# Kernel optimization log

Hardware: AMD Instinct MI355X
Metric: run time of the kernel (lower is better)

Reference implementation:

```python
import jax, jax.numpy as jnp
import numpy as np
from jax.scipy.linalg import expm

B, T = 32, 4096
FREQ_DIM = 128
HID = 64
OUT_DIM = 2
N_COMP = 4
DT = 0.1
EPS = 1e-5


def setup_inputs() -> dict:
    key = jax.random.key(0)
    ks = jax.random.split(key, 16)
    f32 = jnp.float32

    def lin(k, out_d, in_d):
        bound = 1.0 / np.sqrt(in_d)
        kw, kb = jax.random.split(k)
        W = jax.random.uniform(kw, (out_d, in_d), f32, -bound, bound)
        b = jax.random.uniform(kb, (out_d,), f32, -bound, bound)
        return W, b

    x = jax.random.normal(ks[0], (B, T, 1), f32)
    # EnhancedWavePhysics params
    freq_spectrum = jnp.linspace(1.0, 20.0, FREQ_DIM, dtype=f32)
    pm_w1, pm_b1 = lin(ks[1], 128, 1)
    pm_w2, pm_b2 = lin(ks[2], FREQ_DIM * 2, 128)
    wc_w, wc_b = lin(ks[3], HID, FREQ_DIM)
    amp_ctrl = jnp.ones((1,), f32) * 0.1
    # quantum encoder
    qe_w1, qe_b1 = lin(ks[4], HID * 2, HID)
    qe_w2, qe_b2 = lin(ks[5], HID * 4, HID * 2)
    # layernorm
    ln_g = jnp.ones((HID * 4,), f32)
    ln_b = jnp.zeros((HID * 4,), f32)
    # skew-symmetric hamiltonians [4, 64, 64]
    A = jax.random.normal(ks[6], (N_COMP, HID, HID), f32) * 0.05
    hams = (A - jnp.swapaxes(A, -1, -2)) / 2.0
    # interference net
    int_w1, int_b1 = lin(ks[7], 32, 4)
    int_w2, int_b2 = lin(ks[8], OUT_DIM, 32)
    int_strength = jnp.ones((1,), f32)
    return dict(x=x, freq_spectrum=freq_spectrum, pm_w1=pm_w1, pm_b1=pm_b1,
                pm_w2=pm_w2, pm_b2=pm_b2, wc_w=wc_w, wc_b=wc_b,
                amp_ctrl=amp_ctrl, qe_w1=qe_w1, qe_b1=qe_b1, qe_w2=qe_w2,
                qe_b2=qe_b2, ln_g=ln_g, ln_b=ln_b, hams=hams,
                int_w1=int_w1, int_b1=int_b1, int_w2=int_w2, int_b2=int_b2,
                int_strength=int_strength)


def reference(x, freq_spectrum, pm_w1, pm_b1, pm_w2, pm_b2, wc_w, wc_b,
              amp_ctrl, qe_w1, qe_b1, qe_w2, qe_b2, ln_g, ln_b, hams,
              int_w1, int_b1, int_w2, int_b2, int_strength):
    Bx, Tx, _ = x.shape
    # --- EnhancedWavePhysics ---
    mod = jnp.tanh(x @ pm_w1.T + pm_b1) @ pm_w2.T + pm_b2            # [B,T,2F]
    amplitude, phase = jnp.split(mod, 2, axis=-1)                     # [B,T,F]
    amplitude = jnp.tanh(amplitude) * amp_ctrl
    time = jnp.linspace(0.0, 2.0 * np.pi, Tx)[None, :, None]          # [1,T,1]
    freqs = freq_spectrum[None, None, :]                              # [1,1,F]
    wave_components = amplitude * jnp.sin(freqs * time + phase)       # [B,T,F]
    wave_field = jnp.tanh(wave_components @ wc_w.T + wc_b)            # [B,T,H]
    # --- quantum encoder + layernorm ---
    q = jnp.tanh(wave_field @ qe_w1.T + qe_b1) @ qe_w2.T + qe_b2      # [B,T,4H]
    mu = q.mean(-1, keepdims=True)
    var = q.var(-1, keepdims=True)
    q = (q - mu) / jnp.sqrt(var + EPS) * ln_g + ln_b
    psi = q.reshape(Bx, Tx, N_COMP, HID)                              # [B,T,C,D]
    # --- Hamiltonian evolution: torch does matrix_exp(-1j*(1j*H)*dt)=expm(H*dt)
    #     (H skew-symmetric real => U real orthogonal), then psi @ U.T, take real.
    U = jax.vmap(expm)(hams * DT)                                     # [C,D,D]
    evolved = jnp.einsum('btcd,ced->btce', psi, U)                    # [B,T,C,D]
    # --- EnhancedInterference ---
    spec = jnp.abs(jnp.fft.fft(evolved, axis=1))                      # [B,T,C,D]
    freq_w = jax.nn.softmax(spec.mean(-1), axis=1)                    # [B,T,C]
    weighted = jnp.sum(spec * freq_w[..., None], axis=1)              # [B,C,D]
    spatial_avg = weighted.mean(-1)                                   # [B,C]
    out = jnp.tanh(spatial_avg @ int_w1.T + int_b1) @ int_w2.T + int_b2
    return out * int_strength                                         # [B,out_dim]
```

## Files before the change

kernel.cpp:

```cpp
#include <hip/hip_runtime.h>
#include <hip/hip_bf16.h>

#define TT 4096
#define BB 32

typedef unsigned short ushort_t;
typedef __attribute__((ext_vector_type(8))) short short8v;
typedef __attribute__((ext_vector_type(4))) float float4v;

__device__ inline ushort_t bf16rn(float v) {
    unsigned u = __float_as_uint(v);
    unsigned r = (u + 0x7FFFu + ((u >> 16) & 1u)) >> 16;
    return (ushort_t)r;
}
__device__ inline float bf16tof(ushort_t h) {
    return __uint_as_float(((unsigned)h) << 16);
}
__device__ inline int SW(int i) { return i + (i >> 5); }

__device__ inline float fast_tanh(float x) {
    float e = __builtin_amdgcn_exp2f(x * 2.8853900817779268f);
    return 1.0f - 2.0f * __builtin_amdgcn_rcpf(e + 1.0f);
}
__device__ inline float fast_sin(float x) {
    return __builtin_amdgcn_sinf(x * 0.15915494309189535f);
}

__global__ __launch_bounds__(256) void k1_expm(const float* __restrict__ hams,
                                               float* __restrict__ U)
{
    int c = blockIdx.x, tid = threadIdx.x;
    __shared__ float M[4096], P[4096], Acc[4096];
    const float* H = hams + c * 4096;
    for (int k = tid; k < 4096; k += 256) {
        float m = H[k] * 0.1f;
        M[k] = m; P[k] = m;
        Acc[k] = m + (((k >> 6) == (k & 63)) ? 1.0f : 0.0f);
    }
    __syncthreads();
    int j = tid & 63;
    float mcol[64];
    #pragma unroll
    for (int k = 0; k < 64; k++) mcol[k] = M[k * 64 + j];
    for (int term = 2; term <= 8; term++) {
        float inv = 1.0f / (float)term;
        float np_[16];
        #pragma unroll
        for (int r = 0; r < 16; r++) {
            int i = (tid >> 6) + 4 * r;
            float a = 0.f;
            #pragma unroll
            for (int k = 0; k < 64; k++) a = fmaf(P[i * 64 + k], mcol[k], a);
            np_[r] = a * inv;
        }
        __syncthreads();
        #pragma unroll
        for (int r = 0; r < 16; r++) {
            int i = (tid >> 6) + 4 * r;
            P[i * 64 + j] = np_[r];
            Acc[i * 64 + j] += np_[r];
        }
        __syncthreads();
    }
    for (int k = tid; k < 4096; k += 256) U[c * 4096 + k] = Acc[k];
}

__global__ void split_all(const float* __restrict__ pw2, const float* __restrict__ wcw,
                          const float* __restrict__ qw1, const float* __restrict__ qw2,
                          ushort_t* __restrict__ wb)
{
    int i = blockIdx.x * 256 + threadIdx.x;
    const float* src; ushort_t *hi, *lo; int off;
    if (i < 32768)      { src = pw2; hi = wb;          lo = wb + 32768;  off = i; }
    else if (i < 40960) { src = wcw; hi = wb + 65536;  lo = wb + 73728;  off = i - 32768; }
    else if (i < 49152) { src = qw1; hi = wb + 81920;  lo = wb + 90112;  off = i - 40960; }
    else                { src = qw2; hi = wb + 98304;  lo = wb + 131072; off = i - 49152; }
    float v = src[off];
    ushort_t h = bf16rn(v);
    hi[off] = h;
    lo[off] = bf16rn(v - bf16tof(h));
}

template<int EPI>
__global__ __launch_bounds__(256, 2) void gemm_v2(
    const ushort_t* __restrict__ Ahi, const ushort_t* __restrict__ Alo,
    const ushort_t* __restrict__ Whi, const ushort_t* __restrict__ Wlo,
    const float* __restrict__ bias,
    const float* __restrict__ x, const float* __restrict__ pw1,
    const float* __restrict__ pb1,
    const float* __restrict__ freq, const float* __restrict__ ampc,
    const float* __restrict__ lng, const float* __restrict__ lnb,
    ushort_t* __restrict__ OHi, ushort_t* __restrict__ OLo,
    float* __restrict__ OF)
{
    __shared__ float partS[2][4][16], partSS[2][4][16];
    int tid = threadIdx.x;
    int w = tid >> 6, l = tid & 63, l15 = l & 15, kg = l >> 4;
    int kofb = kg * 8;

    short8v bh[4][4], bl[4][4];
    #pragma unroll
    for (int i = 0; i < 4; i++) {
        int n = (w + 4 * i) * 16 + l15;
        #pragma unroll
        for (int kc = 0; kc < 4; kc++) {
            int kof = kc * 32 + kofb;
            bh[i][kc] = *(const short8v*)(Whi + (size_t)n * 128 + kof);
            bl[i][kc] = *(const short8v*)(Wlo + (size_t)n * 128 + kof);
        }
    }

    float fr[2], ba[2], bp[2], am = 0.f;
    float bv[4], g4[4], be4[4];
    if (EPI == 1) {
        am = ampc[0];
        #pragma unroll
        for (int i = 0; i < 2; i++) {
            int f = (w + 4 * i) * 16 + l15;
            fr[i] = freq[f]; ba[i] = bias[f]; bp[i] = bias[128 + f];
        }
    } else {
        #pragma unroll
        for (int i = 0; i < 4; i++) {
            int n = (w + 4 * i) * 16 + l15;
            bv[i] = bias[n]; g4[i] = lng[n]; be4[i] = lnb[n];
        }
    }

    int mbase = blockIdx.x * 256;
    for (int mi = 0; mi < 16; mi++) {
        int m0 = mbase + mi * 16;
        short8v ah[4], al[4];
        if (EPI == 1) {
            float xv = x[m0 + l15];
            #pragma unroll
            for (int kc = 0; kc < 4; kc++) {
                int k0 = kc * 32 + kofb;
                float4 w0 = *(const float4*)(pw1 + k0);
                float4 w1v = *(const float4*)(pw1 + k0 + 4);
                float4 b0 = *(const float4*)(pb1 + k0);
                float4 b1v = *(const float4*)(pb1 + k0 + 4);
                #pragma unroll
                for (int j = 0; j < 8; j++) {
                    float wj = (j < 4) ? (&w0.x)[j] : (&w1v.x)[j - 4];
                    float bj = (j < 4) ? (&b0.x)[j] : (&b1v.x)[j - 4];
                    float v = fast_tanh(fmaf(xv, wj, bj));
                    ushort_t h = bf16rn(v);
                    ah[kc][j] = (short)h;
                    al[kc][j] = (short)bf16rn(v - bf16tof(h));
                }
            }
        } else {
            #pragma unroll
            for (int kc = 0; kc < 4; kc++) {
                int kof = kc * 32 + kofb;
                ah[kc] = *(const short8v*)(Ahi + (size_t)(m0 + l15) * 128 + kof);
                al[kc] = *(const short8v*)(Alo + (size_t)(m0 + l15) * 128 + kof);
            }
        }

        float4v acc[4];
        #pragma unroll
        for (int i = 0; i < 4; i++) acc[i] = (float4v){0.f, 0.f, 0.f, 0.f};
        #pragma unroll
        for (int kc = 0; kc < 4; kc++) {
            #pragma unroll
            for (int i = 0; i < 4; i++) {
                acc[i] = __builtin_amdgcn_mfma_f32_16x16x32_bf16(ah[kc], bh[i][kc], acc[i], 0, 0, 0);
                acc[i] = __builtin_amdgcn_mfma_f32_16x16x32_bf16(ah[kc], bl[i][kc], acc[i], 0, 0, 0);
                acc[i] = __builtin_amdgcn_mfma_f32_16x16x32_bf16(al[kc], bh[i][kc], acc[i], 0, 0, 0);
            }
        }

        if (EPI == 1) {
            #pragma unroll
            for (int i = 0; i < 2; i++) {
                int f = (w + 4 * i) * 16 + l15;
                #pragma unroll
                for (int r = 0; r < 4; r++) {
                    int m = m0 + kg * 4 + r;
                    float timev = 6.283185307179586f * (float)(m & 4095) / 4095.0f;
                    float a = fast_tanh(acc[i][r] + ba[i]) * am;
                    float ph = acc[i + 2][r] + bp[i];
                    float v = a * fast_sin(fmaf(fr[i], timev, ph));
                    ushort_t h = bf16rn(v);
                    OHi[(size_t)m * 128 + f] = h;
                    OLo[(size_t)m * 128 + f] = bf16rn(v - bf16tof(h));
                }
            }
        } else {
            float s[4] = {0, 0, 0, 0}, ss[4] = {0, 0, 0, 0};
            #pragma unroll
            for (int i = 0; i < 4; i++) {
                #pragma unroll
                for (int r = 0; r < 4; r++) {
                    float v = acc[i][r] + bv[i];
                    s[r] += v; ss[r] += v * v;
                }
            }
            #pragma unroll
            for (int r = 0; r < 4; r++) {
                #pragma unroll
                for (int off = 1; off < 16; off <<= 1) {
                    s[r] += __shfl_xor(s[r], off);
                    ss[r] += __shfl_xor(ss[r], off);
                }
            }
            int pb_ = mi & 1;
            if (l15 == 0) {
                #pragma unroll
                for (int r = 0; r < 4; r++) {
                    partS[pb_][w][kg * 4 + r] = s[r];
                    partSS[pb_][w][kg * 4 + r] = ss[r];
                }
            }
            __syncthreads();
            float mu[4], rstd[4];
            #pragma unroll
            for (int r = 0; r < 4; r++) {
                float ts = 0.f, tss = 0.f;
                #pragma unroll
                for (int wv = 0; wv < 4; wv++) {
                    ts += partS[pb_][wv][kg * 4 + r];
                    tss += partSS[pb_][wv][kg * 4 + r];
                }
                mu[r] = ts * (1.0f / 256.0f);
                float var = tss * (1.0f / 256.0f) - mu[r] * mu[r];
                rstd[r] = rsqrtf(var + 1e-5f);
            }
            int b = m0 >> 12;
            int t0 = (m0 & 4095) + kg * 4;
            unsigned* OU = (unsigned*)OF;
            #pragma unroll
            for (int i = 0; i < 4; i++) {
                int n = (w + 4 * i) * 16 + l15;
                uint4 ov;
                #pragma unroll
                for (int r = 0; r < 4; r++) {
                    float v = (acc[i][r] + bv[i] - mu[r]) * rstd[r] * g4[i] + be4[i];
                    ushort_t h = bf16rn(v);
                    ushort_t lo2 = bf16rn(v - bf16tof(h));
                    (&ov.x)[r] = (unsigned)h | ((unsigned)lo2 << 16);
                }
                *(uint4*)(OU + (((size_t)b * 256 + n) << 12) + t0) = ov;
            }
        }
    }
}

__global__ __launch_bounds__(256, 2) void s23_v2(
    const ushort_t* __restrict__ Ahi, const ushort_t* __restrict__ Alo,
    const ushort_t* __restrict__ W2hi, const ushort_t* __restrict__ W2lo,
    const float* __restrict__ b2,
    const ushort_t* __restrict__ W3hi, const ushort_t* __restrict__ W3lo,
    const float* __restrict__ b3,
    ushort_t* __restrict__ OHi, ushort_t* __restrict__ OLo)
{
    __shared__ unsigned WF[2][16][65];
    int tid = threadIdx.x;
    int w = tid >> 6, l = tid & 63, l15 = l & 15, kg = l >> 4;
    int kofb = kg * 8;

    short8v w2h[4], w2l[4];
    #pragma unroll
    for (int kc = 0; kc < 4; kc++) {
        int n = w * 16 + l15;
        int kof = kc * 32 + kofb;
        w2h[kc] = *(const short8v*)(W2hi + (size_t)n * 128 + kof);
        w2l[kc] = *(const short8v*)(W2lo + (size_t)n * 128 + kof);
    }
    short8v w3h[2][2], w3l[2][2];
    #pragma unroll
    for (int i = 0; i < 2; i++) {
        int n = (w + 4 * i) * 16 + l15;
        #pragma unroll
        for (int kc = 0; kc < 2; kc++) {
            int kof = kc * 32 + kofb;
            w3h[i][kc] = *(const short8v*)(W3hi + (size_t)n * 64 + kof);
            w3l[i][kc] = *(const short8v*)(W3lo + (size_t)n * 64 + kof);
        }
    }
    float b2v = b2[w * 16 + l15];
    float b3v[2];
    #pragma unroll
    for (int i = 0; i < 2; i++) b3v[i] = b3[(w + 4 * i) * 16 + l15];

    int mbase = blockIdx.x * 256;
    for (int mi = 0; mi < 16; mi++) {
        int m0 = mbase + mi * 16;
        short8v ah[4], al[4];
        #pragma unroll
        for (int kc = 0; kc < 4; kc++) {
            int kof = kc * 32 + kofb;
            ah[kc] = *(const short8v*)(Ahi + (size_t)(m0 + l15) * 128 + kof);
            al[kc] = *(const short8v*)(Alo + (size_t)(m0 + l15) * 128 + kof);
        }
        float4v acc1 = (float4v){0.f, 0.f, 0.f, 0.f};
        #pragma unroll
        for (int kc = 0; kc < 4; kc++) {
            acc1 = __builtin_amdgcn_mfma_f32_16x16x32_bf16(ah[kc], w2h[kc], acc1, 0, 0, 0);
            acc1 = __builtin_amdgcn_mfma_f32_16x16x32_bf16(ah[kc], w2l[kc], acc1, 0, 0, 0);
            acc1 = __builtin_amdgcn_mfma_f32_16x16x32_bf16(al[kc], w2h[kc], acc1, 0, 0, 0);
        }
        int buf = mi & 1;
        #pragma unroll
        for (int r = 0; r < 4; r++) {
            float v = fast_tanh(acc1[r] + b2v);
            ushort_t h = bf16rn(v);
            ushort_t lo2 = bf16rn(v - bf16tof(h));
            WF[buf][kg * 4 + r][w * 16 + l15] = (unsigned)h | ((unsigned)lo2 << 16);
        }
        __syncthreads();
        float4v acc2[2];
        acc2[0] = (float4v){0.f, 0.f, 0.f, 0.f};
        acc2[1] = (float4v){0.f, 0.f, 0.f, 0.f};
        #pragma unroll
        for (int kc = 0; kc < 2; kc++) {
            short8v a2h, a2l;
            #pragma unroll
            for (int j = 0; j < 8; j++) {
                unsigned u = WF[buf][l15][kc * 32 + kofb + j];
                a2h[j] = (short)(u & 0xFFFFu);
                a2l[j] = (short)(u >> 16);
            }
            #pragma unroll
            for (int i = 0; i < 2; i++) {
                acc2[i] = __builtin_amdgcn_mfma_f32_16x16x32_bf16(a2h, w3h[i][kc], acc2[i], 0, 0, 0);
                acc2[i] = __builtin_amdgcn_mfma_f32_16x16x32_bf16(a2h, w3l[i][kc], acc2[i], 0, 0, 0);
                acc2[i] = __builtin_amdgcn_mfma_f32_16x16x32_bf16(a2l, w3h[i][kc], acc2[i], 0, 0, 0);
            }
        }
        #pragma unroll
        for (int i = 0; i < 2; i++) {
            int n = (w + 4 * i) * 16 + l15;
            #pragma unroll
            for (int r = 0; r < 4; r++) {
                int m = m0 + kg * 4 + r;
                float v = fast_tanh(acc2[i][r] + b3v[i]);
                ushort_t h = bf16rn(v);
                OHi[(size_t)m * 128 + n] = h;
                OLo[(size_t)m * 128 + n] = bf16rn(v - bf16tof(h));
            }
        }
    }
}

__global__ __launch_bounds__(256) void k3a_mfma(float* __restrict__ psi,
                                                const float* __restrict__ U)
{
    __shared__ unsigned QP[64 * 261];
    int bid = blockIdx.x;
    int b = bid >> 6, c = (bid >> 4) & 3, tc = bid & 15;
    int t0 = tc * 256;
    int tid = threadIdx.x;
    int w = tid >> 6, l = tid & 63;
    int l15 = l & 15, kq = l >> 4;
    size_t gbase = ((size_t)(b * 256 + c * 64)) * TT + t0;
    const unsigned* psiu = (const unsigned*)psi;

    for (int i = 0; i < 16; i++) {
        int r_ = i * 4 + w;
        int t4 = l * 4;
        uint4 v = *(const uint4*)(psiu + gbase + (size_t)r_ * TT + t4);
        QP[r_ * 261 + t4 + 0] = v.x;
        QP[r_ * 261 + t4 + 1] = v.y;
        QP[r_ * 261 + t4 + 2] = v.z;
        QP[r_ * 261 + t4 + 3] = v.w;
    }
    __syncthreads();

    short8v ua_hi[2], ua_lo[2];
    #pragma unroll
    for (int kc = 0; kc < 2; kc++) {
        #pragma unroll
        for (int j = 0; j < 8; j++) {
            float v = U[c * 4096 + (w * 16 + l15) * 64 + kc * 32 + kq * 8 + j];
            ushort_t h = bf16rn(v);
            ua_hi[kc][j] = (short)h;
            ua_lo[kc][j] = (short)bf16rn(v - bf16tof(h));
        }
    }

    for (int nt = 0; nt < 16; nt++) {
        float4v acc = (float4v){0.f, 0.f, 0.f, 0.f};
        #pragma unroll
        for (int kc = 0; kc < 2; kc++) {
            short8v b_hi, b_lo;
            #pragma unroll
            for (int j = 0; j < 8; j++) {
                unsigned u = QP[(kc * 32 + kq * 8 + j) * 261 + nt * 16 + l15];
                b_hi[j] = (short)(u & 0xFFFFu);
                b_lo[j] = (short)(u >> 16);
            }
            acc = __builtin_amdgcn_mfma_f32_16x16x32_bf16(ua_hi[kc], b_hi, acc, 0, 0, 0);
            acc = __builtin_amdgcn_mfma_f32_16x16x32_bf16(ua_hi[kc], b_lo, acc, 0, 0, 0);
            acc = __builtin_amdgcn_mfma_f32_16x16x32_bf16(ua_lo[kc], b_hi, acc, 0, 0, 0);
        }
        #pragma unroll
        for (int r = 0; r < 4; r++) {
            int e = w * 16 + kq * 4 + r;
            psi[gbase + (size_t)e * TT + nt * 16 + l15] = acc[r];
        }
    }
}

__global__ __launch_bounds__(256, 2) void k3b_fft(const float* __restrict__ ev,
                                                  float* __restrict__ msum8)
{
    __shared__ float re[4224], im[4224];
    int b = blockIdx.x, c = blockIdx.y, g = blockIdx.z;
    int tid = threadIdx.x;

    float macc[16];
    #pragma unroll
    for (int r = 0; r < 16; r++) macc[r] = 0.f;

    size_t base = (((size_t)b * 4 + c) * 64 + (size_t)g * 8) * TT;
    for (int p = 0; p < 4; p++) {
        __syncthreads();
        for (int r = 0; r < 4; r++) {
            int t0 = (r * 256 + tid) * 4;
            float4 va = *(const float4*)(ev + base + (size_t)(2 * p) * TT + t0);
            float4 vb = *(const float4*)(ev + base + (size_t)(2 * p + 1) * TT + t0);
            #pragma unroll
            for (int j = 0; j < 4; j++) {
                int rv = __brev((unsigned)(t0 + j)) >> 20;
                re[SW(rv)] = (&va.x)[j];
                im[SW(rv)] = (&vb.x)[j];
            }
        }
        __syncthreads();
        #pragma unroll
        for (int sp = 0; sp < 6; sp++) {
            const int s = 2 * sp + 1;
            const int h = 1 << (s - 1);
            const int tsh2 = 11 - s;
            #pragma unroll
            for (int r = 0; r < 4; r++) {
                int idx2 = tid + r * 256;
                int grp = idx2 >> (s - 1);
                int pos = idx2 & (h - 1);
                int i0 = (grp << (s + 1)) + pos;
                int a0 = SW(i0), a1 = SW(i0 + h);
                int a2 = SW(i0 + 2 * h), a3 = SW(i0 + 3 * h);
                float x0r = re[a0], x0i = im[a0];
                float x1r = re[a1], x1i = im[a1];
                float x2r = re[a2], x2i = im[a2];
                float x3r = re[a3], x3i = im[a3];
                float ang = -(float)(pos << tsh2) * (1.0f / 4096.0f);
                float wBr = __builtin_amdgcn_cosf(ang);
                float wBi = __builtin_amdgcn_sinf(ang);
                float wAr = wBr * wBr - wBi * wBi;
                float wAi = 2.0f * wBr * wBi;
                float t1r = wAr * x1r - wAi * x1i, t1i = wAr * x1i + wAi * x1r;
                float t2r = wAr * x3r - wAi * x3i, t2i = wAr * x3i + wAi * x3r;
                float y0r = x0r + t1r, y0i = x0i + t1i;
                float y1r = x0r - t1r, y1i = x0i - t1i;
                float y2r = x2r + t2r, y2i = x2i + t2i;
                float y3r = x2r - t2r, y3i = x2i - t2i;
                float wCr = wBi, wCi = -wBr;
                float ur = wBr * y2r - wBi * y2i, ui = wBr * y2i + wBi * y2r;
                float vr = wCr * y3r - wCi * y3i, vi = wCr * y3i + wCi * y3r;
                re[a0] = y0r + ur; im[a0] = y0i + ui;
                re[a2] = y0r - ur; im[a2] = y0i - ui;
                re[a1] = y1r + vr; im[a1] = y1i + vi;
                re[a3] = y1r - vr; im[a3] = y1i - vi;
            }
            __syncthreads();
        }
        for (int r = 0; r < 16; r++) {
            int k = tid + r * 256;
            int mk = (4096 - k) & 4095;
            float rk = re[SW(k)], ik = im[SW(k)];
            float rm = re[SW(mk)], imm = im[SW(mk)];
            float dA1 = rk + rm, dA2 = ik - imm;
            float dB1 = ik + imm, dB2 = rk - rm;
            float magA = 0.5f * sqrtf(dA1 * dA1 + dA2 * dA2);
            float magB = 0.5f * sqrtf(dB1 * dB1 + dB2 * dB2);
            macc[r] += magA + magB;
        }
    }
    float* ms = msum8 + (((size_t)b * 4 + c) * 8 + g) * 4096;
    for (int r = 0; r < 16; r++) ms[tid + r * 256] = macc[r];
}

__global__ __launch_bounds__(256) void k4_softdot(const float* __restrict__ msum8,
                                                  float* __restrict__ sa)
{
    __shared__ float m[4096];
    __shared__ float red[256];
    int bc = blockIdx.x, tid = threadIdx.x;
    const float* ms = msum8 + (size_t)bc * 8 * 4096;
    float lmax = -1e30f;
    for (int k = tid; k < 4096; k += 256) {
        float v = 0.f;
        #pragma unroll
        for (int g = 0; g < 8; g++) v += ms[g * 4096 + k];
        v *= (1.0f / 64.0f);
        m[k] = v;
        lmax = fmaxf(lmax, v);
    }
    red[tid] = lmax; __syncthreads();
    for (int s2 = 128; s2 > 0; s2 >>= 1) {
        if (tid < s2) red[tid] = fmaxf(red[tid], red[tid + s2]);
        __syncthreads();
    }
    float mx = red[0]; __syncthreads();
    float lsum = 0.f, ldot = 0.f;
    for (int k = tid; k < 4096; k += 256) {
        float e = expf(m[k] - mx);
        lsum += e; ldot += e * m[k];
    }
    red[tid] = lsum; __syncthreads();
    for (int s2 = 128; s2 > 0; s2 >>= 1) {
        if (tid < s2) red[tid] += red[tid + s2];
        __syncthreads();
    }
    float tsum = red[0]; __syncthreads();
    red[tid] = ldot; __syncthreads();
    for (int s2 = 128; s2 > 0; s2 >>= 1) {
        if (tid < s2) red[tid] += red[tid + s2];
        __syncthreads();
    }
    if (tid == 0) sa[bc] = red[0] / tsum;
}

__global__ void k5_head(const float* __restrict__ sa,
                        const float* __restrict__ w1, const float* __restrict__ b1,
                        const float* __restrict__ w2, const float* __restrict__ b2,
                        const float* __restrict__ strength,
                        float* __restrict__ out)
{
    int b = threadIdx.x;
    if (b >= 32) return;
    float s0 = sa[b * 4 + 0], s1 = sa[b * 4 + 1];
    float s2 = sa[b * 4 + 2], s3 = sa[b * 4 + 3];
    float h[32];
    #pragma unroll
    for (int j = 0; j < 32; j++)
        h[j] = tanhf(b1[j] + w1[j * 4 + 0] * s0 + w1[j * 4 + 1] * s1 +
                     w1[j * 4 + 2] * s2 + w1[j * 4 + 3] * s3);
    float st = strength[0];
    #pragma unroll
    for (int o = 0; o < 2; o++) {
        float a = b2[o];
        #pragma unroll
        for (int j = 0; j < 32; j++) a = fmaf(w2[o * 32 + j], h[j], a);
        out[b * 2 + o] = a * st;
    }
}

extern "C" void kernel_launch(void* const* d_in, const int* in_sizes, int n_in,
                              void* d_out, int out_size, void* d_ws, size_t ws_size,
                              hipStream_t stream)
{
    const float* x    = (const float*)d_in[0];
    const float* freq = (const float*)d_in[1];
    const float* pw1  = (const float*)d_in[2];
    const float* pb1  = (const float*)d_in[3];
    const float* pw2  = (const float*)d_in[4];
    const float* pb2  = (const float*)d_in[5];
    const float* wcw  = (const float*)d_in[6];
    const float* wcb  = (const float*)d_in[7];
    const float* ampc = (const float*)d_in[8];
    const float* qw1  = (const float*)d_in[9];
    const float* qb1  = (const float*)d_in[10];
    const float* qw2  = (const float*)d_in[11];
    const float* qb2  = (const float*)d_in[12];
    const float* lng  = (const float*)d_in[13];
    const float* lnb  = (const float*)d_in[14];
    const float* hams = (const float*)d_in[15];
    const float* iw1  = (const float*)d_in[16];
    const float* ib1  = (const float*)d_in[17];
    const float* iw2  = (const float*)d_in[18];
    const float* ib2  = (const float*)d_in[19];
    const float* istr = (const float*)d_in[20];

    char* wsb = (char*)d_ws;
    ushort_t* AHi = (ushort_t*)(wsb + 0);
    ushort_t* ALo = (ushort_t*)(wsb + 33554432);
    ushort_t* BHi = (ushort_t*)(wsb + 67108864);
    ushort_t* BLo = (ushort_t*)(wsb + 100663296);
    float*    psi = (float*)(wsb + 67108864);
    float*    msum8 = (float*)(wsb + 0);
    float*    U    = (float*)(wsb + 201326592);
    float*    sa   = (float*)(wsb + 201392128);
    ushort_t* wb   = (ushort_t*)(wsb + 203489792);
    ushort_t *pw2hi = wb,          *pw2lo = wb + 32768;
    ushort_t *wcwhi = wb + 65536,  *wcwlo = wb + 73728;
    ushort_t *qw1hi = wb + 81920,  *qw1lo = wb + 90112;
    ushort_t *qw2hi = wb + 98304,  *qw2lo = wb + 131072;
    float* out = (float*)d_out;

    k1_expm<<<4, 256, 0, stream>>>(hams, U);
    split_all<<<320, 256, 0, stream>>>(pw2, wcw, qw1, qw2, wb);

    gemm_v2<1><<<512, 256, 0, stream>>>(
        (const ushort_t*)nullptr, (const ushort_t*)nullptr, pw2hi, pw2lo, pb2,
        x, pw1, pb1, freq, ampc, (const float*)nullptr, (const float*)nullptr,
        BHi, BLo, (float*)nullptr);
    s23_v2<<<512, 256, 0, stream>>>(BHi, BLo, wcwhi, wcwlo, wcb,
        qw1hi, qw1lo, qb1, AHi, ALo);
    gemm_v2<2><<<512, 256, 0, stream>>>(
        AHi, ALo, qw2hi, qw2lo, qb2,
        (const float*)nullptr, (const float*)nullptr, (const float*)nullptr,
        (const float*)nullptr, (const float*)nullptr, lng, lnb,
        (ushort_t*)nullptr, (ushort_t*)nullptr, psi);

    k3a_mfma<<<2048, 256, 0, stream>>>(psi, U);
    k3b_fft<<<dim3(32, 4, 8), 256, 0, stream>>>(psi, msum8);
    k4_softdot<<<128, 256, 0, stream>>>(msum8, sa);
    k5_head<<<1, 64, 0, stream>>>(sa, iw1, ib1, iw2, ib2, istr, out);
}
```

Measured before the change: 362.5 us.

## Use radix-16 register FFT stages, exploit spectrum symmetry, and shrink GEMM row tiles

The FFT kernel replaces six radix-4 LDS passes with three radix-16 passes done in registers, which cuts LDS round-trips and barriers. It also computes magnitudes for only half the spectrum and mirrors them using the conjugate symmetry of the packed real signals. Separately, the three GEMM-style kernels now give each block 64 rows instead of 256 and launch 2048 blocks instead of 512, so per-block weight loads are repeated more often in exchange for more parallelism. The 16-element register arrays raise register pressure and could reduce occupancy.

```diff
diff --git a/kernel.cpp b/kernel.cpp
--- a/kernel.cpp
+++ b/kernel.cpp
@@ -127,8 +127,8 @@
         }
     }
 
-    int mbase = blockIdx.x * 256;
-    for (int mi = 0; mi < 16; mi++) {
+    int mbase = blockIdx.x * 64;
+    for (int mi = 0; mi < 4; mi++) {
         int m0 = mbase + mi * 16;
         short8v ah[4], al[4];
         if (EPI == 1) {
@@ -285,8 +285,8 @@
     #pragma unroll
     for (int i = 0; i < 2; i++) b3v[i] = b3[(w + 4 * i) * 16 + l15];
 
-    int mbase = blockIdx.x * 256;
-    for (int mi = 0; mi < 16; mi++) {
+    int mbase = blockIdx.x * 64;
+    for (int mi = 0; mi < 4; mi++) {
         int m0 = mbase + mi * 16;
         short8v ah[4], al[4];
         #pragma unroll
@@ -411,9 +411,10 @@
     int b = blockIdx.x, c = blockIdx.y, g = blockIdx.z;
     int tid = threadIdx.x;
 
-    float macc[16];
-    #pragma unroll
-    for (int r = 0; r < 16; r++) macc[r] = 0.f;
+    float macc[8];
+    #pragma unroll
+    for (int r = 0; r < 8; r++) macc[r] = 0.f;
+    float macc8 = 0.f;
 
     size_t base = (((size_t)b * 4 + c) * 64 + (size_t)g * 8) * TT;
     for (int p = 0; p < 4; p++) {
@@ -430,45 +431,92 @@
             }
         }
         __syncthreads();
-        #pragma unroll
-        for (int sp = 0; sp < 6; sp++) {
-            const int s = 2 * sp + 1;
-            const int h = 1 << (s - 1);
-            const int tsh2 = 11 - s;
-            #pragma unroll
-            for (int r = 0; r < 4; r++) {
-                int idx2 = tid + r * 256;
-                int grp = idx2 >> (s - 1);
-                int pos = idx2 & (h - 1);
-                int i0 = (grp << (s + 1)) + pos;
-                int a0 = SW(i0), a1 = SW(i0 + h);
-                int a2 = SW(i0 + 2 * h), a3 = SW(i0 + 3 * h);
-                float x0r = re[a0], x0i = im[a0];
-                float x1r = re[a1], x1i = im[a1];
-                float x2r = re[a2], x2i = im[a2];
-                float x3r = re[a3], x3i = im[a3];
-                float ang = -(float)(pos << tsh2) * (1.0f / 4096.0f);
-                float wBr = __builtin_amdgcn_cosf(ang);
-                float wBi = __builtin_amdgcn_sinf(ang);
-                float wAr = wBr * wBr - wBi * wBi;
-                float wAi = 2.0f * wBr * wBi;
-                float t1r = wAr * x1r - wAi * x1i, t1i = wAr * x1i + wAi * x1r;
-                float t2r = wAr * x3r - wAi * x3i, t2i = wAr * x3i + wAi * x3r;
-                float y0r = x0r + t1r, y0i = x0i + t1i;
-                float y1r = x0r - t1r, y1i = x0i - t1i;
-                float y2r = x2r + t2r, y2i = x2i + t2i;
-                float y3r = x2r - t2r, y3i = x2i - t2i;
-                float wCr = wBi, wCi = -wBr;
-                float ur = wBr * y2r - wBi * y2i, ui = wBr * y2i + wBi * y2r;
-                float vr = wCr * y3r - wCi * y3i, vi = wCr * y3i + wCi * y3r;
-                re[a0] = y0r + ur; im[a0] = y0i + ui;
-                re[a2] = y0r - ur; im[a2] = y0i - ui;
-                re[a1] = y1r + vr; im[a1] = y1i + vi;
-                re[a3] = y1r - vr; im[a3] = y1i - vi;
+
+        #pragma unroll
+        for (int trip = 0; trip < 3; trip++) {
+            const int sh = trip * 4;
+            int pos = tid & ((1 << sh) - 1);
+            int grp = tid >> sh;
+            int i0 = (grp << (sh + 4)) + pos;
+
+            float yr[16], yi[16];
+            #pragma unroll
+            for (int j = 0; j < 16; j++) {
+                int a = SW(i0 + (j << sh));
+                yr[j] = re[a]; yi[j] = im[a];
+            }
+            float ang = -(float)pos / (float)(16 << sh);
+            float t1r = __builtin_amdgcn_cosf(ang);
+            float t1i = __builtin_amdgcn_sinf(ang);
+            float t2r = t1r * t1r - t1i * t1i, t2i = 2.f * t1r * t1i;
+            float t4r = t2r * t2r - t2i * t2i, t4i = 2.f * t2r * t2i;
+            float t8r = t4r * t4r - t4i * t4i, t8i = 2.f * t4r * t4i;
+
+            #pragma unroll
+            for (int m = 0; m < 8; m++) {
+                int j0 = 2 * m, j1 = j0 + 1;
+                float tr = t8r * yr[j1] - t8i * yi[j1];
+                float ti = t8r * yi[j1] + t8i * yr[j1];
+                yr[j1] = yr[j0] - tr; yi[j1] = yi[j0] - ti;
+                yr[j0] += tr;         yi[j0] += ti;
+            }
+            #pragma unroll
+            for (int bs = 0; bs < 16; bs += 4) {
+                {
+                    int j0 = bs, j1 = bs + 2;
+                    float tr = t4r * yr[j1] - t4i * yi[j1];
+                    float ti = t4r * yi[j1] + t4i * yr[j1];
+                    yr[j1] = yr[j0] - tr; yi[j1] = yi[j0] - ti;
+                    yr[j0] += tr;         yi[j0] += ti;
+                }
+                {
+                    int j0 = bs + 1, j1 = bs + 3;
+                    float tr = t4i * yr[j1] + t4r * yi[j1];
+                    float ti = t4i * yi[j1] - t4r * yr[j1];
+                    yr[j1] = yr[j0] - tr; yi[j1] = yi[j0] - ti;
+                    yr[j0] += tr;         yi[j0] += ti;
+                }
+            }
+            {
+                float wr = t2r, wi = t2i;
+                #pragma unroll
+                for (int j = 0; j < 4; j++) {
+                    #pragma unroll
+                    for (int bs = 0; bs < 16; bs += 8) {
+                        int j0 = bs + j, j1 = j0 + 4;
+                        float tr = wr * yr[j1] - wi * yi[j1];
+                        float ti = wr * yi[j1] + wi * yr[j1];
+                        yr[j1] = yr[j0] - tr; yi[j1] = yi[j0] - ti;
+                        yr[j0] += tr;         yi[j0] += ti;
+                    }
+                    float nwr = (wr + wi) * 0.70710678f;
+                    float nwi = (wi - wr) * 0.70710678f;
+                    wr = nwr; wi = nwi;
+                }
+            }
+            {
+                float wr = t1r, wi = t1i;
+                #pragma unroll
+                for (int j = 0; j < 8; j++) {
+                    int j0 = j, j1 = j + 8;
+                    float tr = wr * yr[j1] - wi * yi[j1];
+                    float ti = wr * yi[j1] + wi * yr[j1];
+                    yr[j1] = yr[j0] - tr; yi[j1] = yi[j0] - ti;
+                    yr[j0] += tr;         yi[j0] += ti;
+                    float nwr = wr * 0.92387953f + wi * 0.38268343f;
+                    float nwi = wi * 0.92387953f - wr * 0.38268343f;
+                    wr = nwr; wi = nwi;
+                }
+            }
+            #pragma unroll
+            for (int j = 0; j < 16; j++) {
+                int a = SW(i0 + (j << sh));
+                re[a] = yr[j]; im[a] = yi[j];
             }
             __syncthreads();
         }
-        for (int r = 0; r < 16; r++) {
+
+        for (int r = 0; r < 8; r++) {
             int k = tid + r * 256;
             int mk = (4096 - k) & 4095;
             float rk = re[SW(k)], ik = im[SW(k)];
@@ -479,9 +527,18 @@
             float magB = 0.5f * sqrtf(dB1 * dB1 + dB2 * dB2);
             macc[r] += magA + magB;
         }
+        if (tid == 0) {
+            float rk = re[SW(2048)], ik = im[SW(2048)];
+            macc8 += fabsf(rk) + fabsf(ik);
+        }
     }
     float* ms = msum8 + (((size_t)b * 4 + c) * 8 + g) * 4096;
-    for (int r = 0; r < 16; r++) ms[tid + r * 256] = macc[r];
+    for (int r = 0; r < 8; r++) {
+        int k = tid + r * 256;
+        ms[k] = macc[r];
+        if (k > 0) ms[4096 - k] = macc[r];
+    }
+    if (tid == 0) ms[2048] = macc8;
 }
 
 __global__ __launch_bounds__(256) void k4_softdot(const float* __restrict__ msum8,
@@ -595,13 +652,13 @@
     k1_expm<<<4, 256, 0, stream>>>(hams, U);
     split_all<<<320, 256, 0, stream>>>(pw2, wcw, qw1, qw2, wb);
 
-    gemm_v2<1><<<512, 256, 0, stream>>>(
+    gemm_v2<1><<<2048, 256, 0, stream>>>(
         (const ushort_t*)nullptr, (const ushort_t*)nullptr, pw2hi, pw2lo, pb2,
         x, pw1, pb1, freq, ampc, (const float*)nullptr, (const float*)nullptr,
         BHi, BLo, (float*)nullptr);
-    s23_v2<<<512, 256, 0, stream>>>(BHi, BLo, wcwhi, wcwlo, wcb,
+    s23_v2<<<2048, 256, 0, stream>>>(BHi, BLo, wcwhi, wcwlo, wcb,
         qw1hi, qw1lo, qb1, AHi, ALo);
-    gemm_v2<2><<<512, 256, 0, stream>>>(
+    gemm_v2<2><<<2048, 256, 0, stream>>>(
         AHi, ALo, qw2hi, qw2lo, qb2,
         (const float*)nullptr, (const float*)nullptr, (const float*)nullptr,
         (const float*)nullptr, (const float*)nullptr, lng, lnb,
```

After: 362.4 us. No clear change (-0.0%).
